# Optimization experiments

Measured on AMD Instinct MI355X. Metric: run time of the kernel, lower is better.

## Reference

```python
import jax, jax.numpy as jnp
import numpy as np

EMBED_DIM = 512
N_HEADS = 8
HEAD_DIM = EMBED_DIM // N_HEADS
B, N = 4, 2048


def setup_inputs() -> dict:
    key = jax.random.key(0)
    ks = jax.random.split(key, 5)
    x = jax.random.normal(ks[0], (B, N, EMBED_DIM), dtype=jnp.float32)
    # torch Linear weights are (out, in); init scale ~ 1/sqrt(in)
    s = 1.0 / np.sqrt(EMBED_DIM)
    WQ = jax.random.uniform(ks[1], (EMBED_DIM, EMBED_DIM), jnp.float32, -s, s)
    WK = jax.random.uniform(ks[2], (EMBED_DIM, EMBED_DIM), jnp.float32, -s, s)
    WV = jax.random.uniform(ks[3], (EMBED_DIM, EMBED_DIM), jnp.float32, -s, s)
    WO = jax.random.uniform(ks[4], (EMBED_DIM, EMBED_DIM), jnp.float32, -s, s)
    mask = jnp.tril(jnp.ones((N, N), dtype=jnp.int32))  # causal mask
    return {"x": x, "WQ": WQ, "WK": WK, "WV": WV, "WO": WO, "mask": mask}


def reference(x, WQ, WK, WV, WO, mask):
    scale = HEAD_DIM ** -0.5
    # Linear: y = x @ W.T ; then split heads -> (B, H, N, Dh)
    def proj(W):
        y = jnp.einsum('bnd,ed->bne', x, W)
        return y.reshape(B, N, N_HEADS, HEAD_DIM).transpose(0, 2, 1, 3)
    Q, K, V = proj(WQ), proj(WK), proj(WV)
    scores = jnp.einsum('bhnd,bhmd->bhnm', Q, K) * scale  # (B,H,N,N)
    scores = jnp.where(mask[None, None, :, :] == 0, -jnp.inf, scores)
    attn = jax.nn.softmax(scores, axis=-1)
    # dropout is identity in eval mode
    out = jnp.einsum('bhnm,bhmd->bhnd', attn, V)
    out = out.transpose(0, 2, 1, 3).reshape(B, N, EMBED_DIM)
    return jnp.einsum('bne,de->bnd', out, WO)
```

## Files before the change

### kernel.cpp

```cpp
#include <hip/hip_runtime.h>
#include <hip/hip_bf16.h>

#define B_  4
#define N_  2048
#define E_  512
#define H_  8
#define DH_ 64
#define M_  (B_ * N_)

typedef __attribute__((ext_vector_type(8))) short bq8;
typedef __attribute__((ext_vector_type(4))) float f32x4;

#define QSCALE_ (0.125f * 1.44269504f)

static __device__ __forceinline__ unsigned short f2bf(float f) {
    unsigned u = __float_as_uint(f);
    unsigned r = (u + 0x7fffu + ((u >> 16) & 1u)) >> 16;
    return (unsigned short)r;
}

static __device__ __forceinline__ unsigned cvtpk_bf16(float lo, float hi) {
    unsigned r;
    asm("v_cvt_pk_bf16_f32 %0, %1, %2" : "=v"(r) : "v"(lo), "v"(hi));
    return r;
}

static __device__ __forceinline__ void gld_lds16(const unsigned short* g,
                                                 unsigned short* l)
{
    __builtin_amdgcn_global_load_lds(
        (const __attribute__((address_space(1))) void*)g,
        (__attribute__((address_space(3))) void*)l,
        16, 0, 0);
}

static __device__ __forceinline__ void cvt16(const void* src, unsigned short* dst,
                                             int base, bool isBf)
{
    if (isBf) {
        const uint4* s = (const uint4*)((const unsigned short*)src + base);
        uint4 a = s[0], b = s[1];
        *(uint4*)(dst + base)     = a;
        *(uint4*)(dst + base + 8) = b;
    } else {
        const float* s = (const float*)src + base;
        unsigned short tmp[16];
        #pragma unroll
        for (int c = 0; c < 16; c += 4) {
            const float4 v = *(const float4*)(s + c);
            tmp[c + 0] = f2bf(v.x); tmp[c + 1] = f2bf(v.y);
            tmp[c + 2] = f2bf(v.z); tmp[c + 3] = f2bf(v.w);
        }
        *(uint4*)(dst + base)     = *(uint4*)&tmp[0];
        *(uint4*)(dst + base + 8) = *(uint4*)&tmp[8];
    }
}

__global__ __launch_bounds__(256)
void cvt_all(const void* __restrict__ sx,
             const void* __restrict__ s0, const void* __restrict__ s1,
             const void* __restrict__ s2, const void* __restrict__ s3,
             unsigned short* __restrict__ dx,
             unsigned short* __restrict__ d0, unsigned short* __restrict__ d1,
             unsigned short* __restrict__ d2, unsigned short* __restrict__ d3,
             int* __restrict__ dflag)
{
    __shared__ int wtot[4];
    const int bid = blockIdx.x;
    const int t   = threadIdx.x;
    const void* s;
    unsigned short* d;
    int base;
    if (bid < 1024) {
        s = sx; d = dx;
        base = bid * 4096 + t * 16;
    } else {
        const int wb = bid - 1024;
        const int wi = wb >> 6;
        s = (wi == 0) ? s0 : (wi == 1) ? s1 : (wi == 2) ? s2 : s3;
        d = (wi == 0) ? d0 : (wi == 1) ? d1 : (wi == 2) ? d2 : d3;
        base = (wb & 63) * 4096 + t * 16;
    }

    const unsigned* sw = (const unsigned*)s;
    int cnt = 0;
    #pragma unroll
    for (int i = 0; i < 4; ++i) {
        const unsigned w = sw[t * 4 + i];
        const unsigned elo = (w >> 7) & 0xffu;
        const unsigned ehi = (w >> 23) & 0xffu;
        cnt += (elo >= 100u && elo <= 150u && ehi >= 100u && ehi <= 150u) ? 1 : 0;
    }
    cnt += __shfl_xor(cnt, 1);  cnt += __shfl_xor(cnt, 2);
    cnt += __shfl_xor(cnt, 4);  cnt += __shfl_xor(cnt, 8);
    cnt += __shfl_xor(cnt, 16); cnt += __shfl_xor(cnt, 32);
    if ((t & 63) == 0) wtot[t >> 6] = cnt;
    __syncthreads();
    const int total = wtot[0] + wtot[1] + wtot[2] + wtot[3];
    const bool isBf = (total >= 512);
    if (bid == 0 && t == 0) dflag[0] = isBf ? 1 : 0;

    cvt16(s, d, base, isBf);
}

template<int BN>
__global__ __launch_bounds__(256)
void gemm_bf16(const unsigned short* __restrict__ A,
               const unsigned short* __restrict__ W0,
               const unsigned short* __restrict__ W1,
               const unsigned short* __restrict__ W2,
               void* __restrict__ C0, void* __restrict__ C1, void* __restrict__ C2,
               const int* __restrict__ dflag, int cSel)
{
    constexpr int NB = BN / 32;
    __shared__ unsigned short As[2][128 * 32];
    __shared__ unsigned short Bs[2][BN * 32];

    const int extBf = dflag[0];
    const unsigned short* Wv = (blockIdx.z == 0) ? W0 : (blockIdx.z == 1) ? W1 : W2;
    void*                 Cv = (blockIdx.z == 0) ? C0 : (blockIdx.z == 1) ? C1 : C2;
    const int  mode  = (cSel == 1) ? 1 : ((blockIdx.z == 2) ? 2 : 0);
    const bool vswap = (mode == 2);
    const float qs = (cSel == 0 && blockIdx.z == 0) ? QSCALE_ : 1.0f;

    const int t    = threadIdx.x;
    const int w    = t >> 6;
    const int lane = t & 63;
    const int ln   = lane & 15;
    const int qd   = lane >> 4;
    const int wm   = w >> 1;
    const int wn   = w & 1;

    const int m0 = blockIdx.x * 128;
    const int n0 = blockIdx.y * BN;

    const int lr = lane >> 2;
    const int lc = (lane & 3) * 8;
    const unsigned short* gA0 = A + (size_t)(m0 + w * 32 + lr) * E_ + lc;
    const unsigned short* gA1 = gA0 + 16 * E_;
    const int aOff0 = w * 32 * 32;
    const int aOff1 = aOff0 + 16 * 32;

    const unsigned short* gB0;
    const unsigned short* gB1 = nullptr;
    int bOff0, bOff1 = 0;
    if (BN == 128) {
        gB0 = Wv + (size_t)(n0 + w * 32 + lr) * E_ + lc;
        gB1 = gB0 + 16 * E_;
        bOff0 = w * 32 * 32;
        bOff1 = bOff0 + 16 * 32;
    } else {
        gB0 = Wv + (size_t)(n0 + w * 16 + lr) * E_ + lc;
        bOff0 = w * 16 * 32;
    }

    f32x4 acc[4][4];
    #pragma unroll
    for (int i = 0; i < 4; ++i)
        #pragma unroll
        for (int j = 0; j < 4; ++j)
            acc[i][j] = (f32x4){0.f, 0.f, 0.f, 0.f};

    for (int k0 = 0; k0 < E_; k0 += 64) {
        __syncthreads();
        gld_lds16(gA0 + k0,      &As[0][aOff0]);
        gld_lds16(gA1 + k0,      &As[0][aOff1]);
        gld_lds16(gA0 + k0 + 32, &As[1][aOff0]);
        gld_lds16(gA1 + k0 + 32, &As[1][aOff1]);
        gld_lds16(gB0 + k0,      &Bs[0][bOff0]);
        gld_lds16(gB0 + k0 + 32, &Bs[1][bOff0]);
        if (BN == 128) {
            gld_lds16(gB1 + k0,      &Bs[0][bOff1]);
            gld_lds16(gB1 + k0 + 32, &Bs[1][bOff1]);
        }
        __syncthreads();

        #pragma unroll
        for (int half = 0; half < 2; ++half) {
            bq8 afr[4], bfr[NB];
            #pragma unroll
            for (int i = 0; i < 4; ++i)
                afr[i] = *(const bq8*)&As[half][(wm * 64 + i * 16 + ln) * 32 + qd * 8];
            #pragma unroll
            for (int j = 0; j < NB; ++j)
                bfr[j] = *(const bq8*)&Bs[half][(wn * (BN / 2) + j * 16 + ln) * 32 + qd * 8];

            if (vswap) {
                #pragma unroll
                for (int i = 0; i < 4; ++i)
                    #pragma unroll
                    for (int j = 0; j < NB; ++j)
                        acc[i][j] = __builtin_amdgcn_mfma_f32_16x16x32_bf16(afr[i], bfr[j], acc[i][j], 0, 0, 0);
            } else {
                #pragma unroll
                for (int i = 0; i < NB; ++i)
                    #pragma unroll
                    for (int j = 0; j < 4; ++j)
                        acc[i][j] = __builtin_amdgcn_mfma_f32_16x16x32_bf16(bfr[i], afr[j], acc[i][j], 0, 0, 0);
            }
        }
    }

    if (mode == 2) {
        unsigned short* C = (unsigned short*)Cv;
        const int colBase = n0 + wn * 64;
        const int hh = colBase >> 6;
        #pragma unroll
        for (int i = 0; i < 4; ++i) {
            const int token = m0 + wm * 64 + i * 16 + qd * 4;
            const int bb = token >> 11;
            const int nn = token & 2047;
            #pragma unroll
            for (int j = 0; j < 4; ++j) {
                const int d = j * 16 + ln;
                ushort4 o4;
                o4.x = f2bf(acc[i][j][0]);
                o4.y = f2bf(acc[i][j][1]);
                o4.z = f2bf(acc[i][j][2]);
                o4.w = f2bf(acc[i][j][3]);
                *(ushort4*)(C + ((size_t)(bb * H_ + hh) * 64 + d) * N_ + nn) = o4;
            }
        }
    } else if (mode == 0 || extBf) {
        unsigned short* C = (unsigned short*)Cv;
        #pragma unroll
        for (int i = 0; i < NB; ++i) {
            const int n = n0 + wn * (BN / 2) + i * 16 + qd * 4;
            #pragma unroll
            for (int j = 0; j < 4; ++j) {
                const int m = m0 + wm * 64 + j * 16 + ln;
                ushort4 o4;
                o4.x = f2bf(acc[i][j][0] * qs);
                o4.y = f2bf(acc[i][j][1] * qs);
                o4.z = f2bf(acc[i][j][2] * qs);
                o4.w = f2bf(acc[i][j][3] * qs);
                *(ushort4*)(C + (size_t)m * E_ + n) = o4;
            }
        }
    } else {
        float* C = (float*)Cv;
        #pragma unroll
        for (int i = 0; i < NB; ++i) {
            const int n = n0 + wn * (BN / 2) + i * 16 + qd * 4;
            #pragma unroll
            for (int j = 0; j < 4; ++j) {
                const int m = m0 + wm * 64 + j * 16 + ln;
                *(f32x4*)(C + (size_t)m * E_ + n) = acc[i][j];
            }
        }
    }
}

__global__ __launch_bounds__(256)
void attn_causal(const unsigned short* __restrict__ Q,
                 const unsigned short* __restrict__ K,
                 const unsigned short* __restrict__ VtG,
                 unsigned short* __restrict__ O)
{
    __shared__ unsigned short Ks[128 * 72];
    __shared__ unsigned short Vs[64 * 136];
    __shared__ unsigned short Pq[64 * 136];

    const int bx  = blockIdx.x;
    const int qlo = bx;
    const int qhi = 31 - bx;
    const int h   = blockIdx.y;
    const int b   = blockIdx.z;
    const int t   = threadIdx.x;
    const int w    = t >> 6;
    const int lane = t & 63;
    const int ln   = lane & 15;
    const int qd   = lane >> 4;

    const int CA = (qlo + 2) >> 1;
    const int CB = (qhi + 2) >> 1;

    const int col0 = h * DH_;
    const size_t rowBase = (size_t)b * N_;
    const unsigned short* Vhead = VtG + (size_t)(b * H_ + h) * 64 * N_;

    const int jbase = qd * 4;
    const int mloc  = w * 16 + ln;
    const int qAg = qlo * 64 + mloc;
    const int qBg = qhi * 64 + mloc;
    const int prow = mloc * 136;

    const unsigned short* Qa = Q + (rowBase + qAg) * E_ + col0 + qd * 8;
    const unsigned short* Qb = Q + (rowBase + qBg) * E_ + col0 + qd * 8;
    const bq8 qfA0 = *(const bq8*)(Qa);
    const bq8 qfA1 = *(const bq8*)(Qa + 32);
    const bq8 qfB0 = *(const bq8*)(Qb);
    const bq8 qfB1 = *(const bq8*)(Qb + 32);

    const int kr = t >> 1;
    const int kc = (t & 1) * 32;
    const int vr = t >> 2;
    const int vc = (t & 3) * 32;
    const unsigned short* gK = K + (rowBase + kr) * E_ + col0 + kc;
    const unsigned short* gV = Vhead + (size_t)vr * N_ + vc;

    float lA = 0.f, lB = 0.f;
    f32x4 oA[4], oB[4];
    #pragma unroll
    for (int dt = 0; dt < 4; ++dt) {
        oA[dt] = (f32x4){0.f, 0.f, 0.f, 0.f};
        oB[dt] = (f32x4){0.f, 0.f, 0.f, 0.f};
    }

    uint4 kR0, kR1, kR2, kR3, vR0, vR1, vR2, vR3;
    {
        const uint4* ks = (const uint4*)gK;
        kR0 = ks[0]; kR1 = ks[1]; kR2 = ks[2]; kR3 = ks[3];
        const uint4* vs = (const uint4*)gV;
        vR0 = vs[0]; vR1 = vs[1]; vR2 = vs[2]; vR3 = vs[3];
    }

    for (int kt = 0; kt < CB; ++kt) {
        __syncthreads();
        *(uint4*)&Ks[kr * 72 + kc]      = kR0;
        *(uint4*)&Ks[kr * 72 + kc + 8]  = kR1;
        *(uint4*)&Ks[kr * 72 + kc + 16] = kR2;
        *(uint4*)&Ks[kr * 72 + kc + 24] = kR3;
        *(uint4*)&Vs[vr * 136 + vc]      = vR0;
        *(uint4*)&Vs[vr * 136 + vc + 8]  = vR1;
        *(uint4*)&Vs[vr * 136 + vc + 16] = vR2;
        *(uint4*)&Vs[vr * 136 + vc + 24] = vR3;
        __syncthreads();

        if (kt + 1 < CB) {
            const uint4* ks = (const uint4*)(gK + (size_t)(kt + 1) * 128 * E_);
            kR0 = ks[0]; kR1 = ks[1]; kR2 = ks[2]; kR3 = ks[3];
            const uint4* vs = (const uint4*)(gV + (kt + 1) * 128);
            vR0 = vs[0]; vR1 = vs[1]; vR2 = vs[2]; vR3 = vs[3];
        }

        const int gb = kt * 128 + jbase;

        if (kt < CA) {
            const bool diagA = (kt == CA - 1);
            f32x4 sB[8];
            #pragma unroll
            for (int ct = 0; ct < 8; ++ct) {
                const bq8 kf0 = *(const bq8*)&Ks[(ct * 16 + ln) * 72 + qd * 8];
                const bq8 kf1 = *(const bq8*)&Ks[(ct * 16 + ln) * 72 + 32 + qd * 8];
                __builtin_amdgcn_s_setprio(1);
                f32x4 ca = (f32x4){0.f, 0.f, 0.f, 0.f};
                ca = __builtin_amdgcn_mfma_f32_16x16x32_bf16(kf0, qfA0, ca, 0, 0, 0);
                ca = __builtin_amdgcn_mfma_f32_16x16x32_bf16(kf1, qfA1, ca, 0, 0, 0);
                f32x4 c = (f32x4){0.f, 0.f, 0.f, 0.f};
                c = __builtin_amdgcn_mfma_f32_16x16x32_bf16(kf0, qfB0, c, 0, 0, 0);
                c = __builtin_amdgcn_mfma_f32_16x16x32_bf16(kf1, qfB1, c, 0, 0, 0);
                __builtin_amdgcn_s_setprio(0);
                sB[ct] = c;
                float p0 = exp2f(ca[0]);
                float p1 = exp2f(ca[1]);
                float p2 = exp2f(ca[2]);
                float p3 = exp2f(ca[3]);
                if (diagA) {
                    const int kb = gb + ct * 16;
                    if (kb + 0 > qAg) p0 = 0.f;
                    if (kb + 1 > qAg) p1 = 0.f;
                    if (kb + 2 > qAg) p2 = 0.f;
                    if (kb + 3 > qAg) p3 = 0.f;
                }
                lA += (p0 + p1) + (p2 + p3);
                uint2 pk2;
                pk2.x = cvtpk_bf16(p0, p1);
                pk2.y = cvtpk_bf16(p2, p3);
                *(uint2*)&Pq[prow + ct * 16 + jbase] = pk2;
            }
            const bq8 pA0 = *(const bq8*)&Pq[prow + qd * 8];
            const bq8 pA1 = *(const bq8*)&Pq[prow + 32 + qd * 8];
            const bq8 pA2 = *(const bq8*)&Pq[prow + 64 + qd * 8];
            const bq8 pA3 = *(const bq8*)&Pq[prow + 96 + qd * 8];

            #pragma unroll
            for (int ct = 0; ct < 8; ++ct) {
                const float p0 = exp2f(sB[ct][0]);
                const float p1 = exp2f(sB[ct][1]);
                const float p2 = exp2f(sB[ct][2]);
                const float p3 = exp2f(sB[ct][3]);
                lB += (p0 + p1) + (p2 + p3);
                uint2 pk2;
                pk2.x = cvtpk_bf16(p0, p1);
                pk2.y = cvtpk_bf16(p2, p3);
                *(uint2*)&Pq[prow + ct * 16 + jbase] = pk2;
            }
            const bq8 pB0 = *(const bq8*)&Pq[prow + qd * 8];
            const bq8 pB1 = *(const bq8*)&Pq[prow + 32 + qd * 8];
            const bq8 pB2 = *(const bq8*)&Pq[prow + 64 + qd * 8];
            const bq8 pB3 = *(const bq8*)&Pq[prow + 96 + qd * 8];

            __builtin_amdgcn_s_setprio(1);
            #pragma unroll
            for (int dt = 0; dt < 4; ++dt) {
                const int vb = (dt * 16 + ln) * 136;
                const bq8 vf0 = *(const bq8*)&Vs[vb + qd * 8];
                const bq8 vf1 = *(const bq8*)&Vs[vb + 32 + qd * 8];
                const bq8 vf2 = *(const bq8*)&Vs[vb + 64 + qd * 8];
                const bq8 vf3 = *(const bq8*)&Vs[vb + 96 + qd * 8];
                oB[dt] = __builtin_amdgcn_mfma_f32_16x16x32_bf16(vf0, pB0, oB[dt], 0, 0, 0);
                oB[dt] = __builtin_amdgcn_mfma_f32_16x16x32_bf16(vf1, pB1, oB[dt], 0, 0, 0);
                oB[dt] = __builtin_amdgcn_mfma_f32_16x16x32_bf16(vf2, pB2, oB[dt], 0, 0, 0);
                oB[dt] = __builtin_amdgcn_mfma_f32_16x16x32_bf16(vf3, pB3, oB[dt], 0, 0, 0);
                oA[dt] = __builtin_amdgcn_mfma_f32_16x16x32_bf16(vf0, pA0, oA[dt], 0, 0, 0);
                oA[dt] = __builtin_amdgcn_mfma_f32_16x16x32_bf16(vf1, pA1, oA[dt], 0, 0, 0);
                oA[dt] = __builtin_amdgcn_mfma_f32_16x16x32_bf16(vf2, pA2, oA[dt], 0, 0, 0);
                oA[dt] = __builtin_amdgcn_mfma_f32_16x16x32_bf16(vf3, pA3, oA[dt], 0, 0, 0);
            }
            __builtin_amdgcn_s_setprio(0);
        } else {
            const bool diagB = (kt == CB - 1);
            #pragma unroll
            for (int ct = 0; ct < 8; ++ct) {
                const bq8 kf0 = *(const bq8*)&Ks[(ct * 16 + ln) * 72 + qd * 8];
                const bq8 kf1 = *(const bq8*)&Ks[(ct * 16 + ln) * 72 + 32 + qd * 8];
                __builtin_amdgcn_s_setprio(1);
                f32x4 c = (f32x4){0.f, 0.f, 0.f, 0.f};
                c = __builtin_amdgcn_mfma_f32_16x16x32_bf16(kf0, qfB0, c, 0, 0, 0);
                c = __builtin_amdgcn_mfma_f32_16x16x32_bf16(kf1, qfB1, c, 0, 0, 0);
                __builtin_amdgcn_s_setprio(0);
                float p0 = exp2f(c[0]);
                float p1 = exp2f(c[1]);
                float p2 = exp2f(c[2]);
                float p3 = exp2f(c[3]);
                if (diagB) {
                    const int kb = gb + ct * 16;
                    if (kb + 0 > qBg) p0 = 0.f;
                    if (kb + 1 > qBg) p1 = 0.f;
                    if (kb + 2 > qBg) p2 = 0.f;
                    if (kb + 3 > qBg) p3 = 0.f;
                }
                lB += (p0 + p1) + (p2 + p3);
                uint2 pk2;
                pk2.x = cvtpk_bf16(p0, p1);
                pk2.y = cvtpk_bf16(p2, p3);
                *(uint2*)&Pq[prow + ct * 16 + jbase] = pk2;
            }
            const bq8 pB0 = *(const bq8*)&Pq[prow + qd * 8];
            const bq8 pB1 = *(const bq8*)&Pq[prow + 32 + qd * 8];
            const bq8 pB2 = *(const bq8*)&Pq[prow + 64 + qd * 8];
            const bq8 pB3 = *(const bq8*)&Pq[prow + 96 + qd * 8];

            __builtin_amdgcn_s_setprio(1);
            #pragma unroll
            for (int dt = 0; dt < 4; ++dt) {
                const int vb = (dt * 16 + ln) * 136;
                const bq8 vf0 = *(const bq8*)&Vs[vb + qd * 8];
                const bq8 vf1 = *(const bq8*)&Vs[vb + 32 + qd * 8];
                const bq8 vf2 = *(const bq8*)&Vs[vb + 64 + qd * 8];
                const bq8 vf3 = *(const bq8*)&Vs[vb + 96 + qd * 8];
                oB[dt] = __builtin_amdgcn_mfma_f32_16x16x32_bf16(vf0, pB0, oB[dt], 0, 0, 0);
                oB[dt] = __builtin_amdgcn_mfma_f32_16x16x32_bf16(vf1, pB1, oB[dt], 0, 0, 0);
                oB[dt] = __builtin_amdgcn_mfma_f32_16x16x32_bf16(vf2, pB2, oB[dt], 0, 0, 0);
                oB[dt] = __builtin_amdgcn_mfma_f32_16x16x32_bf16(vf3, pB3, oB[dt], 0, 0, 0);
            }
            __builtin_amdgcn_s_setprio(0);
        }
    }

    lA += __shfl_xor(lA, 16); lA += __shfl_xor(lA, 32);
    lB += __shfl_xor(lB, 16); lB += __shfl_xor(lB, 32);
    const float invA = 1.f / lA;
    const float invB = 1.f / lB;

    unsigned short* oAp = O + (rowBase + qlo * 64 + mloc) * E_ + col0 + jbase;
    unsigned short* oBp = O + (rowBase + qhi * 64 + mloc) * E_ + col0 + jbase;
    #pragma unroll
    for (int dt = 0; dt < 4; ++dt) {
        uint2 a2, b2;
        a2.x = cvtpk_bf16(oA[dt][0] * invA, oA[dt][1] * invA);
        a2.y = cvtpk_bf16(oA[dt][2] * invA, oA[dt][3] * invA);
        b2.x = cvtpk_bf16(oB[dt][0] * invB, oB[dt][1] * invB);
        b2.y = cvtpk_bf16(oB[dt][2] * invB, oB[dt][3] * invB);
        *(uint2*)(oAp + dt * 16) = a2;
        *(uint2*)(oBp + dt * 16) = b2;
    }
}

extern "C" void kernel_launch(void* const* d_in, const int* in_sizes, int n_in,
                              void* d_out, int out_size, void* d_ws, size_t ws_size,
                              hipStream_t stream)
{
    const void* x  = d_in[0];
    const void* WQ = d_in[1];
    const void* WK = d_in[2];
    const void* WV = d_in[3];
    const void* WO = d_in[4];

    int* dflag = (int*)d_ws;
    unsigned short* xb  = (unsigned short*)((char*)d_ws + 256);
    unsigned short* wqb = xb  + (size_t)M_ * E_;
    unsigned short* wkb = wqb + (size_t)E_ * E_;
    unsigned short* wvb = wkb + (size_t)E_ * E_;
    unsigned short* wob = wvb + (size_t)E_ * E_;
    unsigned short* q   = wob + (size_t)E_ * E_;
    unsigned short* k   = q   + (size_t)M_ * E_;
    unsigned short* v   = k   + (size_t)M_ * E_;
    unsigned short* o   = v   + (size_t)M_ * E_;

    cvt_all<<<1280, 256, 0, stream>>>(x, WQ, WK, WV, WO,
                                      xb, wqb, wkb, wvb, wob, dflag);

    gemm_bf16<128><<<dim3(M_ / 128, E_ / 128, 3), 256, 0, stream>>>(
        xb, wqb, wkb, wvb, q, k, v, dflag, 0);

    attn_causal<<<dim3(16, H_, B_), 256, 0, stream>>>(q, k, v, o);

    gemm_bf16<64><<<dim3(M_ / 128, E_ / 64, 1), 256, 0, stream>>>(
        o, wob, wob, wob, d_out, d_out, d_out, dflag, 1);
}
```

Measured before the change: 170.9 us.

## Pair adjacent query tiles per block with longest-first 1D grid scheduling

Replaces the symmetric pairing of query tiles (i, 31-i) with adjacent tiles (2i, 2i+1) that share the same causal key range. The A/B branching is removed so every iteration processes both tiles with a single masked diagonal step. Blocks are launched on a 1D grid ordered from longest to shortest to soften load imbalance. This trades uniform per-block work for simpler control flow and shared K/V reuse, at the cost of some wasted compute on the fully masked half of the diagonal tile for the lower query tile.

```diff
diff --git a/kernel.cpp b/kernel.cpp
--- a/kernel.cpp
+++ b/kernel.cpp
@@ -261,19 +261,20 @@
     __shared__ unsigned short Vs[64 * 136];
     __shared__ unsigned short Pq[64 * 136];
 
-    const int bx  = blockIdx.x;
-    const int qlo = bx;
-    const int qhi = 31 - bx;
-    const int h   = blockIdx.y;
-    const int b   = blockIdx.z;
+    const int id  = blockIdx.x;
+    const int i   = 15 - (id >> 5);
+    const int hb  = id & 31;
+    const int h   = hb & 7;
+    const int b   = hb >> 3;
+    const int qlo = 2 * i;
+    const int qhi = 2 * i + 1;
+    const int CC  = i + 1;
+
     const int t   = threadIdx.x;
     const int w    = t >> 6;
     const int lane = t & 63;
     const int ln   = lane & 15;
     const int qd   = lane >> 4;
-
-    const int CA = (qlo + 2) >> 1;
-    const int CB = (qhi + 2) >> 1;
 
     const int col0 = h * DH_;
     const size_t rowBase = (size_t)b * N_;
@@ -315,7 +316,7 @@
         vR0 = vs[0]; vR1 = vs[1]; vR2 = vs[2]; vR3 = vs[3];
     }
 
-    for (int kt = 0; kt < CB; ++kt) {
+    for (int kt = 0; kt < CC; ++kt) {
         __syncthreads();
         *(uint4*)&Ks[kr * 72 + kc]      = kR0;
         *(uint4*)&Ks[kr * 72 + kc + 8]  = kR1;
@@ -327,7 +328,7 @@
         *(uint4*)&Vs[vr * 136 + vc + 24] = vR3;
         __syncthreads();
 
-        if (kt + 1 < CB) {
+        if (kt + 1 < CC) {
             const uint4* ks = (const uint4*)(gK + (size_t)(kt + 1) * 128 * E_);
             kR0 = ks[0]; kR1 = ks[1]; kR2 = ks[2]; kR3 = ks[3];
             const uint4* vs = (const uint4*)(gV + (kt + 1) * 128);
@@ -335,128 +336,86 @@
         }
 
         const int gb = kt * 128 + jbase;
-
-        if (kt < CA) {
-            const bool diagA = (kt == CA - 1);
-            f32x4 sB[8];
-            #pragma unroll
-            for (int ct = 0; ct < 8; ++ct) {
-                const bq8 kf0 = *(const bq8*)&Ks[(ct * 16 + ln) * 72 + qd * 8];
-                const bq8 kf1 = *(const bq8*)&Ks[(ct * 16 + ln) * 72 + 32 + qd * 8];
-                __builtin_amdgcn_s_setprio(1);
-                f32x4 ca = (f32x4){0.f, 0.f, 0.f, 0.f};
-                ca = __builtin_amdgcn_mfma_f32_16x16x32_bf16(kf0, qfA0, ca, 0, 0, 0);
-                ca = __builtin_amdgcn_mfma_f32_16x16x32_bf16(kf1, qfA1, ca, 0, 0, 0);
-                f32x4 c = (f32x4){0.f, 0.f, 0.f, 0.f};
-                c = __builtin_amdgcn_mfma_f32_16x16x32_bf16(kf0, qfB0, c, 0, 0, 0);
-                c = __builtin_amdgcn_mfma_f32_16x16x32_bf16(kf1, qfB1, c, 0, 0, 0);
-                __builtin_amdgcn_s_setprio(0);
-                sB[ct] = c;
-                float p0 = exp2f(ca[0]);
-                float p1 = exp2f(ca[1]);
-                float p2 = exp2f(ca[2]);
-                float p3 = exp2f(ca[3]);
-                if (diagA) {
-                    const int kb = gb + ct * 16;
-                    if (kb + 0 > qAg) p0 = 0.f;
-                    if (kb + 1 > qAg) p1 = 0.f;
-                    if (kb + 2 > qAg) p2 = 0.f;
-                    if (kb + 3 > qAg) p3 = 0.f;
-                }
-                lA += (p0 + p1) + (p2 + p3);
-                uint2 pk2;
-                pk2.x = cvtpk_bf16(p0, p1);
-                pk2.y = cvtpk_bf16(p2, p3);
-                *(uint2*)&Pq[prow + ct * 16 + jbase] = pk2;
-            }
-            const bq8 pA0 = *(const bq8*)&Pq[prow + qd * 8];
-            const bq8 pA1 = *(const bq8*)&Pq[prow + 32 + qd * 8];
-            const bq8 pA2 = *(const bq8*)&Pq[prow + 64 + qd * 8];
-            const bq8 pA3 = *(const bq8*)&Pq[prow + 96 + qd * 8];
-
-            #pragma unroll
-            for (int ct = 0; ct < 8; ++ct) {
-                const float p0 = exp2f(sB[ct][0]);
-                const float p1 = exp2f(sB[ct][1]);
-                const float p2 = exp2f(sB[ct][2]);
-                const float p3 = exp2f(sB[ct][3]);
-                lB += (p0 + p1) + (p2 + p3);
-                uint2 pk2;
-                pk2.x = cvtpk_bf16(p0, p1);
-                pk2.y = cvtpk_bf16(p2, p3);
-                *(uint2*)&Pq[prow + ct * 16 + jbase] = pk2;
-            }
-            const bq8 pB0 = *(const bq8*)&Pq[prow + qd * 8];
-            const bq8 pB1 = *(const bq8*)&Pq[prow + 32 + qd * 8];
-            const bq8 pB2 = *(const bq8*)&Pq[prow + 64 + qd * 8];
-            const bq8 pB3 = *(const bq8*)&Pq[prow + 96 + qd * 8];
-
+        const bool diag = (kt == CC - 1);
+
+        f32x4 sB[8];
+        #pragma unroll
+        for (int ct = 0; ct < 8; ++ct) {
+            const bq8 kf0 = *(const bq8*)&Ks[(ct * 16 + ln) * 72 + qd * 8];
+            const bq8 kf1 = *(const bq8*)&Ks[(ct * 16 + ln) * 72 + 32 + qd * 8];
             __builtin_amdgcn_s_setprio(1);
-            #pragma unroll
-            for (int dt = 0; dt < 4; ++dt) {
-                const int vb = (dt * 16 + ln) * 136;
-                const bq8 vf0 = *(const bq8*)&Vs[vb + qd * 8];
-                const bq8 vf1 = *(const bq8*)&Vs[vb + 32 + qd * 8];
-                const bq8 vf2 = *(const bq8*)&Vs[vb + 64 + qd * 8];
-                const bq8 vf3 = *(const bq8*)&Vs[vb + 96 + qd * 8];
-                oB[dt] = __builtin_amdgcn_mfma_f32_16x16x32_bf16(vf0, pB0, oB[dt], 0, 0, 0);
-                oB[dt] = __builtin_amdgcn_mfma_f32_16x16x32_bf16(vf1, pB1, oB[dt], 0, 0, 0);
-                oB[dt] = __builtin_amdgcn_mfma_f32_16x16x32_bf16(vf2, pB2, oB[dt], 0, 0, 0);
-                oB[dt] = __builtin_amdgcn_mfma_f32_16x16x32_bf16(vf3, pB3, oB[dt], 0, 0, 0);
-                oA[dt] = __builtin_amdgcn_mfma_f32_16x16x32_bf16(vf0, pA0, oA[dt], 0, 0, 0);
-                oA[dt] = __builtin_amdgcn_mfma_f32_16x16x32_bf16(vf1, pA1, oA[dt], 0, 0, 0);
-                oA[dt] = __builtin_amdgcn_mfma_f32_16x16x32_bf16(vf2, pA2, oA[dt], 0, 0, 0);
-                oA[dt] = __builtin_amdgcn_mfma_f32_16x16x32_bf16(vf3, pA3, oA[dt], 0, 0, 0);
-            }
+            f32x4 ca = (f32x4){0.f, 0.f, 0.f, 0.f};
+            ca = __builtin_amdgcn_mfma_f32_16x16x32_bf16(kf0, qfA0, ca, 0, 0, 0);
+            ca = __builtin_amdgcn_mfma_f32_16x16x32_bf16(kf1, qfA1, ca, 0, 0, 0);
+            f32x4 c = (f32x4){0.f, 0.f, 0.f, 0.f};
+            c = __builtin_amdgcn_mfma_f32_16x16x32_bf16(kf0, qfB0, c, 0, 0, 0);
+            c = __builtin_amdgcn_mfma_f32_16x16x32_bf16(kf1, qfB1, c, 0, 0, 0);
             __builtin_amdgcn_s_setprio(0);
-        } else {
-            const bool diagB = (kt == CB - 1);
-            #pragma unroll
-            for (int ct = 0; ct < 8; ++ct) {
-                const bq8 kf0 = *(const bq8*)&Ks[(ct * 16 + ln) * 72 + qd * 8];
-                const bq8 kf1 = *(const bq8*)&Ks[(ct * 16 + ln) * 72 + 32 + qd * 8];
-                __builtin_amdgcn_s_setprio(1);
-                f32x4 c = (f32x4){0.f, 0.f, 0.f, 0.f};
-                c = __builtin_amdgcn_mfma_f32_16x16x32_bf16(kf0, qfB0, c, 0, 0, 0);
-                c = __builtin_amdgcn_mfma_f32_16x16x32_bf16(kf1, qfB1, c, 0, 0, 0);
-                __builtin_amdgcn_s_setprio(0);
-                float p0 = exp2f(c[0]);
-                float p1 = exp2f(c[1]);
-                float p2 = exp2f(c[2]);
-                float p3 = exp2f(c[3]);
-                if (diagB) {
-                    const int kb = gb + ct * 16;
-                    if (kb + 0 > qBg) p0 = 0.f;
-                    if (kb + 1 > qBg) p1 = 0.f;
-                    if (kb + 2 > qBg) p2 = 0.f;
-                    if (kb + 3 > qBg) p3 = 0.f;
-                }
-                lB += (p0 + p1) + (p2 + p3);
-                uint2 pk2;
-                pk2.x = cvtpk_bf16(p0, p1);
-                pk2.y = cvtpk_bf16(p2, p3);
-                *(uint2*)&Pq[prow + ct * 16 + jbase] = pk2;
-            }
-            const bq8 pB0 = *(const bq8*)&Pq[prow + qd * 8];
-            const bq8 pB1 = *(const bq8*)&Pq[prow + 32 + qd * 8];
-            const bq8 pB2 = *(const bq8*)&Pq[prow + 64 + qd * 8];
-            const bq8 pB3 = *(const bq8*)&Pq[prow + 96 + qd * 8];
-
-            __builtin_amdgcn_s_setprio(1);
-            #pragma unroll
-            for (int dt = 0; dt < 4; ++dt) {
-                const int vb = (dt * 16 + ln) * 136;
-                const bq8 vf0 = *(const bq8*)&Vs[vb + qd * 8];
-                const bq8 vf1 = *(const bq8*)&Vs[vb + 32 + qd * 8];
-                const bq8 vf2 = *(const bq8*)&Vs[vb + 64 + qd * 8];
-                const bq8 vf3 = *(const bq8*)&Vs[vb + 96 + qd * 8];
-                oB[dt] = __builtin_amdgcn_mfma_f32_16x16x32_bf16(vf0, pB0, oB[dt], 0, 0, 0);
-                oB[dt] = __builtin_amdgcn_mfma_f32_16x16x32_bf16(vf1, pB1, oB[dt], 0, 0, 0);
-                oB[dt] = __builtin_amdgcn_mfma_f32_16x16x32_bf16(vf2, pB2, oB[dt], 0, 0, 0);
-                oB[dt] = __builtin_amdgcn_mfma_f32_16x16x32_bf16(vf3, pB3, oB[dt], 0, 0, 0);
-            }
-            __builtin_amdgcn_s_setprio(0);
-        }
+            sB[ct] = c;
+            float p0 = exp2f(ca[0]);
+            float p1 = exp2f(ca[1]);
+            float p2 = exp2f(ca[2]);
+            float p3 = exp2f(ca[3]);
+            if (diag) {
+                const int kb = gb + ct * 16;
+                if (kb + 0 > qAg) p0 = 0.f;
+                if (kb + 1 > qAg) p1 = 0.f;
+                if (kb + 2 > qAg) p2 = 0.f;
+                if (kb + 3 > qAg) p3 = 0.f;
+            }
+            lA += (p0 + p1) + (p2 + p3);
+            uint2 pk2;
+            pk2.x = cvtpk_bf16(p0, p1);
+            pk2.y = cvtpk_bf16(p2, p3);
+            *(uint2*)&Pq[prow + ct * 16 + jbase] = pk2;
+        }
+        const bq8 pA0 = *(const bq8*)&Pq[prow + qd * 8];
+        const bq8 pA1 = *(const bq8*)&Pq[prow + 32 + qd * 8];
+        const bq8 pA2 = *(const bq8*)&Pq[prow + 64 + qd * 8];
+        const bq8 pA3 = *(const bq8*)&Pq[prow + 96 + qd * 8];
+
+        #pragma unroll
+        for (int ct = 0; ct < 8; ++ct) {
+            float p0 = exp2f(sB[ct][0]);
+            float p1 = exp2f(sB[ct][1]);
+            float p2 = exp2f(sB[ct][2]);
+            float p3 = exp2f(sB[ct][3]);
+            if (diag) {
+                const int kb = gb + ct * 16;
+                if (kb + 0 > qBg) p0 = 0.f;
+                if (kb + 1 > qBg) p1 = 0.f;
+                if (kb + 2 > qBg) p2 = 0.f;
+                if (kb + 3 > qBg) p3 = 0.f;
+            }
+            lB += (p0 + p1) + (p2 + p3);
+            uint2 pk2;
+            pk2.x = cvtpk_bf16(p0, p1);
+            pk2.y = cvtpk_bf16(p2, p3);
+            *(uint2*)&Pq[prow + ct * 16 + jbase] = pk2;
+        }
+        const bq8 pB0 = *(const bq8*)&Pq[prow + qd * 8];
+        const bq8 pB1 = *(const bq8*)&Pq[prow + 32 + qd * 8];
+        const bq8 pB2 = *(const bq8*)&Pq[prow + 64 + qd * 8];
+        const bq8 pB3 = *(const bq8*)&Pq[prow + 96 + qd * 8];
+
+        __builtin_amdgcn_s_setprio(1);
+        #pragma unroll
+        for (int dt = 0; dt < 4; ++dt) {
+            const int vb = (dt * 16 + ln) * 136;
+            const bq8 vf0 = *(const bq8*)&Vs[vb + qd * 8];
+            const bq8 vf1 = *(const bq8*)&Vs[vb + 32 + qd * 8];
+            const bq8 vf2 = *(const bq8*)&Vs[vb + 64 + qd * 8];
+            const bq8 vf3 = *(const bq8*)&Vs[vb + 96 + qd * 8];
+            oB[dt] = __builtin_amdgcn_mfma_f32_16x16x32_bf16(vf0, pB0, oB[dt], 0, 0, 0);
+            oB[dt] = __builtin_amdgcn_mfma_f32_16x16x32_bf16(vf1, pB1, oB[dt], 0, 0, 0);
+            oB[dt] = __builtin_amdgcn_mfma_f32_16x16x32_bf16(vf2, pB2, oB[dt], 0, 0, 0);
+            oB[dt] = __builtin_amdgcn_mfma_f32_16x16x32_bf16(vf3, pB3, oB[dt], 0, 0, 0);
+            oA[dt] = __builtin_amdgcn_mfma_f32_16x16x32_bf16(vf0, pA0, oA[dt], 0, 0, 0);
+            oA[dt] = __builtin_amdgcn_mfma_f32_16x16x32_bf16(vf1, pA1, oA[dt], 0, 0, 0);
+            oA[dt] = __builtin_amdgcn_mfma_f32_16x16x32_bf16(vf2, pA2, oA[dt], 0, 0, 0);
+            oA[dt] = __builtin_amdgcn_mfma_f32_16x16x32_bf16(vf3, pA3, oA[dt], 0, 0, 0);
+        }
+        __builtin_amdgcn_s_setprio(0);
     }
 
     lA += __shfl_xor(lA, 16); lA += __shfl_xor(lA, 32);
@@ -505,7 +464,7 @@
     gemm_bf16<128><<<dim3(M_ / 128, E_ / 128, 3), 256, 0, stream>>>(
         xb, wqb, wkb, wvb, q, k, v, dflag, 0);
 
-    attn_causal<<<dim3(16, H_, B_), 256, 0, stream>>>(q, k, v, o);
+    attn_causal<<<512, 256, 0, stream>>>(q, k, v, o);
 
     gemm_bf16<64><<<dim3(M_ / 128, E_ / 64, 1), 256, 0, stream>>>(
         o, wob, wob, wob, d_out, d_out, d_out, dflag, 1);
```

New measurement: 171.7 us. No clear change (+0.5%).
